# Performance work log

Hardware: AMD Instinct MI355X
Metric: run time of the kernel (lower is better)

Reference implementation:

```python
import jax, jax.numpy as jnp
import numpy as np

B, S, H, E, I_E, V = 4, 4096, 1024, 8, 512, 100000


def setup_inputs() -> dict:
    key = jax.random.key(0)
    k0, k1, k2, k3, k4, k5, k6 = jax.random.split(key, 7)
    hidden_states = jax.random.normal(k0, (B, S, H), dtype=jnp.float32)
    token_ids = jax.random.randint(k1, (B, S), 0, V, dtype=jnp.int64)
    mu = jax.random.normal(k2, (B, S, H), dtype=jnp.float32)
    # torch Linear(in,out,bias=False) weight is [out,in]; we store transposed [in,out]
    w_gate = jax.random.normal(k3, (E, H, I_E), dtype=jnp.float32) * 0.02
    w_up = jax.random.normal(k4, (E, H, I_E), dtype=jnp.float32) * 0.02
    w_down = jax.random.normal(k5, (E, I_E, H), dtype=jnp.float32) * 0.02
    # module zero-inits mu_router; use small random so the mu-override path is exercised
    mu_router_w = jax.random.normal(k6, (E, H), dtype=jnp.float32) * 0.02
    return {
        "hidden_states": hidden_states,
        "token_ids": token_ids,
        "mu": mu,
        "w_gate": w_gate,
        "w_up": w_up,
        "w_down": w_down,
        "mu_router_w": mu_router_w,
    }


def reference(hidden_states, token_ids, mu, w_gate, w_up, w_down, mu_router_w):
    num_experts = w_gate.shape[0]
    # deterministic token->expert mapping: token_id % num_experts (after clamp)
    tid = jnp.clip(token_ids, 0, V - 1)
    base_expert_ids = (tid % num_experts).astype(jnp.int32)  # [B,S]
    # mu-guided override: one_hot*10 + mu_logits, argmax
    mu_logits = jnp.einsum("bsh,eh->bse", mu, mu_router_w)
    base_one_hot = jax.nn.one_hot(base_expert_ids, num_experts, dtype=mu_logits.dtype)
    expert_ids = jnp.argmax(base_one_hot * 10.0 + mu_logits, axis=-1)  # [B,S]

    x = hidden_states.reshape(-1, H)          # [T,H], T=B*S
    eid = expert_ids.reshape(-1)              # [T]
    out = jnp.zeros_like(x)
    for e in range(num_experts):
        mask = (eid == e)[:, None]            # [T,1]
        g = x @ w_gate[e]                     # [T,I_E]
        u = x @ w_up[e]                       # [T,I_E]
        y = (jax.nn.silu(g) * u) @ w_down[e]  # [T,H] SwiGLU
        out = out + jnp.where(mask, y, 0.0)
    return out.reshape(hidden_states.shape)
```

## Files before the change

### kernel.cpp

```cpp
#include <hip/hip_runtime.h>
#include <stdint.h>

#define T_TOK   16384
#define H_DIM   1024
#define IE_DIM  512
#define E_NUM   8
#define V_MAX   100000

typedef __attribute__((ext_vector_type(8))) short bf16x8;
typedef __attribute__((ext_vector_type(4))) float f32x4;
typedef unsigned long long ull;

__device__ __forceinline__ unsigned short f2bf(float f) {
  union { float f; unsigned u; } v; v.f = f;
  unsigned r = v.u + 0x7fffu + ((v.u >> 16) & 1u);
  return (unsigned short)(r >> 16);
}

__device__ __forceinline__ void gload16(const void* g, void* l) {
  __builtin_amdgcn_global_load_lds(
      (const __attribute__((address_space(1))) unsigned int*)g,
      (__attribute__((address_space(3))) unsigned int*)(unsigned int)(uintptr_t)l,
      16, 0, 0);
}

__global__ __launch_bounds__(256) void k_route(
    const float* __restrict__ mu, const int* __restrict__ tok,
    const float* __restrict__ mrw, int* __restrict__ eid,
    int* __restrict__ blockCnt) {
  __shared__ int cnt[8];
  int tid = threadIdx.x;
  if (tid < 8) cnt[tid] = 0;
  int wv = blockIdx.x * 4 + (tid >> 6);
  int t0 = wv * 4;
  int lane = tid & 63;
  const float4* mrw4 = (const float4*)mrw;

  float acc[4][E_NUM];
#pragma unroll
  for (int i = 0; i < 4; i++)
#pragma unroll
    for (int e = 0; e < E_NUM; e++) acc[i][e] = 0.f;

#pragma unroll
  for (int j = 0; j < 4; j++) {
    int idx = lane + 64 * j;
    float4 wr[E_NUM];
#pragma unroll
    for (int e = 0; e < E_NUM; e++) wr[e] = mrw4[e * 256 + idx];
#pragma unroll
    for (int i = 0; i < 4; i++) {
      float4 m = ((const float4*)(mu + (size_t)(t0 + i) * H_DIM))[idx];
#pragma unroll
      for (int e = 0; e < E_NUM; e++)
        acc[i][e] += m.x * wr[e].x + m.y * wr[e].y + m.z * wr[e].z + m.w * wr[e].w;
    }
  }
#pragma unroll
  for (int i = 0; i < 4; i++)
#pragma unroll
    for (int e = 0; e < E_NUM; e++)
#pragma unroll
      for (int off = 32; off >= 1; off >>= 1)
        acc[i][e] += __shfl_xor(acc[i][e], off, 64);

  __syncthreads();
#pragma unroll
  for (int i = 0; i < 4; i++) {
    int tv = tok[t0 + i];
    if (tv < 0) tv = 0;
    if (tv > V_MAX - 1) tv = V_MAX - 1;
    int base = tv & 7;
    int best = 0; float bs = -1e30f;
#pragma unroll
    for (int e = 0; e < E_NUM; e++) {
      float s = acc[i][e] + (e == base ? 10.f : 0.f);
      if (s > bs) { bs = s; best = e; }
    }
    if (lane == i) {
      eid[t0 + i] = best;
      atomicAdd(&cnt[best], 1);
    }
  }
  __syncthreads();
  if (tid < 8) blockCnt[blockIdx.x * 8 + tid] = cnt[tid];
}

__global__ __launch_bounds__(1024) void k_scan2(
    const int* __restrict__ blockCnt, int* __restrict__ blockBase,
    int* __restrict__ offsets, int* __restrict__ tileOff) {
  int b = threadIdx.x;
  __shared__ ull s0[1024], s1[1024];
  __shared__ int offL[8];
  const int4* p = (const int4*)(blockCnt + b * 8);
  int4 x0 = p[0], x1 = p[1];
  int c[8] = {x0.x, x0.y, x0.z, x0.w, x1.x, x1.y, x1.z, x1.w};
  ull v0 = (ull)c[0] | ((ull)c[1] << 16) | ((ull)c[2] << 32) | ((ull)c[3] << 48);
  ull v1 = (ull)c[4] | ((ull)c[5] << 16) | ((ull)c[6] << 32) | ((ull)c[7] << 48);
  s0[b] = v0; s1[b] = v1;
  __syncthreads();
  for (int st = 1; st < 1024; st <<= 1) {
    ull a0 = 0, a1 = 0;
    if (b >= st) { a0 = s0[b - st]; a1 = s1[b - st]; }
    __syncthreads();
    v0 += a0; v1 += a1;
    s0[b] = v0; s1[b] = v1;
    __syncthreads();
  }
  if (b == 1023) {
    int tot[8];
#pragma unroll
    for (int e = 0; e < 4; e++) tot[e] = (int)((v0 >> (16 * e)) & 0xFFFF);
#pragma unroll
    for (int e = 0; e < 4; e++) tot[4 + e] = (int)((v1 >> (16 * e)) & 0xFFFF);
    int s = 0, ts = 0;
    for (int e = 0; e < E_NUM; e++) {
      offsets[e] = s; offL[e] = s; tileOff[e] = ts;
      s += tot[e];
      ts += (tot[e] + 127) >> 7;
    }
    offsets[E_NUM] = s; tileOff[E_NUM] = ts;
  }
  __syncthreads();
  int be[8];
#pragma unroll
  for (int e = 0; e < 4; e++)
    be[e] = offL[e] + (int)((v0 >> (16 * e)) & 0xFFFF) - c[e];
#pragma unroll
  for (int e = 0; e < 4; e++)
    be[4 + e] = offL[4 + e] + (int)((v1 >> (16 * e)) & 0xFFFF) - c[4 + e];
  int4* q = (int4*)(blockBase + b * 8);
  q[0] = make_int4(be[0], be[1], be[2], be[3]);
  q[1] = make_int4(be[4], be[5], be[6], be[7]);
}

__global__ __launch_bounds__(256) void k_gathtr(
    const float* __restrict__ hs, const int* __restrict__ eid,
    const int* __restrict__ blockBase, int* __restrict__ tokofrow,
    unsigned short* __restrict__ Xs,
    const float* __restrict__ wg, const float* __restrict__ wu,
    const float* __restrict__ wd, unsigned short* __restrict__ WgT,
    unsigned short* __restrict__ WuT, unsigned short* __restrict__ WdT) {
  __shared__ unsigned short lds[64][72];
  int tid = threadIdx.x;

  if (blockIdx.x < 1024) {
    int b = blockIdx.x;
    int* eL = (int*)&lds[0][0];
    int* posL = eL + 16;
    if (tid < 16) eL[tid] = eid[b * 16 + tid];
    __syncthreads();
    if (tid < 16) {
      int e = eL[tid];
      int r = 0;
      for (int j = 0; j < tid; j++) r += (eL[j] == e);
      int pos = blockBase[b * 8 + e] + r;
      posL[tid] = pos;
      tokofrow[pos] = b * 16 + tid;
    }
    __syncthreads();
    int w = tid >> 6, lane = tid & 63;
#pragma unroll
    for (int i = 0; i < 4; i++) {
      int li = w * 4 + i;
      int t = b * 16 + li;
      int pos = posL[li];
      const float4* src = (const float4*)(hs + (size_t)t * H_DIM);
      unsigned short* drow = Xs + (size_t)pos * H_DIM;
#pragma unroll
      for (int j = 0; j < 4; j++) {
        float4 v = src[lane + 64 * j];
        ushort4 bb;
        bb.x = f2bf(v.x); bb.y = f2bf(v.y); bb.z = f2bf(v.z); bb.w = f2bf(v.w);
        *(ushort4*)(drow + (lane + 64 * j) * 4) = bb;
      }
    }
  } else {
    int sel = (blockIdx.x - 1024) >> 10;
    int blk = blockIdx.x & 1023;
    const float* src; unsigned short* dst; int R, C;
    if (sel == 0)      { src = wg; dst = WgT; R = H_DIM; C = IE_DIM; }
    else if (sel == 1) { src = wu; dst = WuT; R = H_DIM; C = IE_DIM; }
    else               { src = wd; dst = WdT; R = IE_DIM; C = H_DIM; }
    int tpe = (R >> 6) * (C >> 6);
    int e = blk / tpe;
    int rem = blk % tpe;
    int tr = rem / (C >> 6);
    int tc = rem % (C >> 6);
    const float* s = src + (size_t)e * R * C;
    unsigned short* d = dst + (size_t)e * R * C;
    int r0 = tid >> 4;
    int c0 = (tid & 15) * 4;
#pragma unroll
    for (int i = 0; i < 4; i++) {
      int r = r0 + i * 16;
      float4 v = *(const float4*)(s + (size_t)(tr * 64 + r) * C + tc * 64 + c0);
      lds[r][c0 + 0] = f2bf(v.x); lds[r][c0 + 1] = f2bf(v.y);
      lds[r][c0 + 2] = f2bf(v.z); lds[r][c0 + 3] = f2bf(v.w);
    }
    __syncthreads();
    int oc = tid >> 2;
    int ob = (tid & 3) * 16;
    unsigned short tmp[16];
#pragma unroll
    for (int i = 0; i < 16; i++) tmp[i] = lds[ob + i][oc];
    uint4* dp = (uint4*)(d + (size_t)(tc * 64 + oc) * R + tr * 64 + ob);
    dp[0] = ((uint4*)tmp)[0];
    dp[1] = ((uint4*)tmp)[1];
  }
}

__global__ __launch_bounds__(512) void k_gemm1(
    const unsigned short* __restrict__ Xs,
    const unsigned short* __restrict__ WgT,
    const unsigned short* __restrict__ WuT,
    unsigned short* __restrict__ Hb,
    const int* __restrict__ offsets, const int* __restrict__ tileOff) {
  int bid0 = blockIdx.x;
  int xcd = bid0 & 7, seq = bid0 >> 3;
  int wg = (xcd < 4 ? xcd * 68 : 272 + (xcd - 4) * 67) + seq;
  int nt = wg & 3;
  int mlin = wg >> 2;
  if (mlin >= tileOff[E_NUM]) return;
  int e = 0;
#pragma unroll
  for (int i = 1; i < E_NUM; i++)
    if (mlin >= tileOff[i]) e = i;
  int mtile = mlin - tileOff[e];
  int segStart = offsets[e], segEnd = offsets[e + 1];
  int M = segEnd - segStart;

  __shared__ unsigned short Alds[3][128 * 32];
  __shared__ unsigned short Bglds[3][128 * 32];
  __shared__ unsigned short Bulds[3][128 * 32];

  int tid = threadIdx.x;
  int lane = tid & 63;
  int w = tid >> 6;
  int wm = w >> 2;
  int wn = w & 3;

  f32x4 accg[4][2], accu[4][2];
#pragma unroll
  for (int i = 0; i < 4; i++)
#pragma unroll
    for (int j = 0; j < 2; j++) {
      accg[i][j] = (f32x4)(0.f);
      accu[i][j] = (f32x4)(0.f);
    }

  int sr = tid >> 2;
  int sc = tid & 3;
  int scc = sc ^ ((sr >> 1) & 3);
  int grow = mtile * 128 + sr;
  if (grow > M - 1) grow = M - 1;
  const unsigned short* Arow = Xs + (size_t)(segStart + grow) * H_DIM + scc * 8;
  const unsigned short* Bgrow =
      WgT + (size_t)e * IE_DIM * H_DIM + (size_t)(nt * 128 + sr) * H_DIM + scc * 8;
  const unsigned short* Burow =
      WuT + (size_t)e * IE_DIM * H_DIM + (size_t)(nt * 128 + sr) * H_DIM + scc * 8;

#define STAGE1(buf, k0)                                            \
  {                                                                \
    gload16(Arow + (k0), (char*)Alds[buf] + tid * 16);             \
    gload16(Bgrow + (k0), (char*)Bglds[buf] + tid * 16);           \
    gload16(Burow + (k0), (char*)Bulds[buf] + tid * 16);           \
  }

  int kc = lane >> 4;
  int arow[4], browv[2];
#pragma unroll
  for (int mf = 0; mf < 4; mf++) arow[mf] = wm * 64 + mf * 16 + (lane & 15);
#pragma unroll
  for (int nf = 0; nf < 2; nf++) browv[nf] = wn * 32 + nf * 16 + (lane & 15);

  const int NT = H_DIM / 32;
  STAGE1(0, 0);
  STAGE1(1, 32);

  int cur = 0;
  for (int t = 0; t < NT; t++) {
    asm volatile("s_waitcnt vmcnt(3)" ::: "memory");
    __builtin_amdgcn_s_barrier();
    __builtin_amdgcn_sched_barrier(0);
    int tn = t + 2; if (tn >= NT) tn -= NT;
    int nbuf = cur + 2; if (nbuf >= 3) nbuf -= 3;
    STAGE1(nbuf, tn * 32);

    bf16x8 a[4], bg[2], bu[2];
#pragma unroll
    for (int mf = 0; mf < 4; mf++) {
      int row = arow[mf];
      int byte = row * 64 + ((kc ^ ((row >> 1) & 3)) << 4);
      a[mf] = *(const bf16x8*)((const char*)Alds[cur] + byte);
    }
#pragma unroll
    for (int nf = 0; nf < 2; nf++) {
      int row = browv[nf];
      int byte = row * 64 + ((kc ^ ((row >> 1) & 3)) << 4);
      bg[nf] = *(const bf16x8*)((const char*)Bglds[cur] + byte);
      bu[nf] = *(const bf16x8*)((const char*)Bulds[cur] + byte);
    }
    __builtin_amdgcn_s_setprio(1);
#pragma unroll
    for (int mf = 0; mf < 4; mf++)
#pragma unroll
      for (int nf = 0; nf < 2; nf++) {
        accg[mf][nf] = __builtin_amdgcn_mfma_f32_16x16x32_bf16(
            a[mf], bg[nf], accg[mf][nf], 0, 0, 0);
        accu[mf][nf] = __builtin_amdgcn_mfma_f32_16x16x32_bf16(
            a[mf], bu[nf], accu[mf][nf], 0, 0, 0);
      }
    __builtin_amdgcn_s_setprio(0);
    cur = (cur + 1 == 3) ? 0 : cur + 1;
  }
#undef STAGE1
  asm volatile("s_waitcnt vmcnt(0)" ::: "memory");

  int rowBase = segStart + mtile * 128 + wm * 64;
#pragma unroll
  for (int mf = 0; mf < 4; mf++)
#pragma unroll
    for (int nf = 0; nf < 2; nf++) {
      int col = nt * 128 + wn * 32 + nf * 16 + (lane & 15);
#pragma unroll
      for (int j = 0; j < 4; j++) {
        int r = rowBase + mf * 16 + (lane >> 4) * 4 + j;
        if (r < segEnd) {
          float g = accg[mf][nf][j];
          float u = accu[mf][nf][j];
          float h = (g / (1.f + __expf(-g))) * u;
          Hb[(size_t)r * IE_DIM + col] = f2bf(h);
        }
      }
    }
}

__global__ __launch_bounds__(512) void k_gemm2(
    const unsigned short* __restrict__ Hb,
    const unsigned short* __restrict__ WdT,
    float* __restrict__ out,
    const int* __restrict__ offsets, const int* __restrict__ tileOff,
    const int* __restrict__ tokofrow) {
  int bid0 = blockIdx.x;
  int wg = (bid0 & 7) * 135 + (bid0 >> 3);
  int nt = wg & 7;
  int mlin = wg >> 3;
  if (mlin >= tileOff[E_NUM]) return;
  int e = 0;
#pragma unroll
  for (int i = 1; i < E_NUM; i++)
    if (mlin >= tileOff[i]) e = i;
  int mtile = mlin - tileOff[e];
  int segStart = offsets[e], segEnd = offsets[e + 1];
  int M = segEnd - segStart;

  __shared__ unsigned short Alds[3][128 * 32];
  __shared__ unsigned short Blds[3][128 * 32];

  int tid = threadIdx.x;
  int lane = tid & 63;
  int w = tid >> 6;
  int wm = w >> 2;
  int wn = w & 3;

  f32x4 acc[4][2];
#pragma unroll
  for (int i = 0; i < 4; i++)
#pragma unroll
    for (int j = 0; j < 2; j++) acc[i][j] = (f32x4)(0.f);

  int sr = tid >> 2;
  int sc = tid & 3;
  int scc = sc ^ ((sr >> 1) & 3);
  int grow = mtile * 128 + sr;
  if (grow > M - 1) grow = M - 1;
  const unsigned short* Arow = Hb + (size_t)(segStart + grow) * IE_DIM + scc * 8;
  const unsigned short* Brow =
      WdT + (size_t)e * H_DIM * IE_DIM + (size_t)(nt * 128 + sr) * IE_DIM + scc * 8;

#define STAGE2(buf, k0)                                            \
  {                                                                \
    gload16(Arow + (k0), (char*)Alds[buf] + tid * 16);             \
    gload16(Brow + (k0), (char*)Blds[buf] + tid * 16);             \
  }

  int kc = lane >> 4;
  int arow[4], browv[2];
#pragma unroll
  for (int mf = 0; mf < 4; mf++) arow[mf] = wm * 64 + mf * 16 + (lane & 15);
#pragma unroll
  for (int nf = 0; nf < 2; nf++) browv[nf] = wn * 32 + nf * 16 + (lane & 15);

  const int NT = IE_DIM / 32;
  STAGE2(0, 0);
  STAGE2(1, 32);

  int cur = 0;
  for (int t = 0; t < NT; t++) {
    asm volatile("s_waitcnt vmcnt(2)" ::: "memory");
    __builtin_amdgcn_s_barrier();
    __builtin_amdgcn_sched_barrier(0);
    int tn = t + 2; if (tn >= NT) tn -= NT;
    int nbuf = cur + 2; if (nbuf >= 3) nbuf -= 3;
    STAGE2(nbuf, tn * 32);

    bf16x8 a[4], b[2];
#pragma unroll
    for (int mf = 0; mf < 4; mf++) {
      int row = arow[mf];
      int byte = row * 64 + ((kc ^ ((row >> 1) & 3)) << 4);
      a[mf] = *(const bf16x8*)((const char*)Alds[cur] + byte);
    }
#pragma unroll
    for (int nf = 0; nf < 2; nf++) {
      int row = browv[nf];
      int byte = row * 64 + ((kc ^ ((row >> 1) & 3)) << 4);
      b[nf] = *(const bf16x8*)((const char*)Blds[cur] + byte);
    }
    __builtin_amdgcn_s_setprio(1);
#pragma unroll
    for (int mf = 0; mf < 4; mf++)
#pragma unroll
      for (int nf = 0; nf < 2; nf++)
        acc[mf][nf] = __builtin_amdgcn_mfma_f32_16x16x32_bf16(
            a[mf], b[nf], acc[mf][nf], 0, 0, 0);
    __builtin_amdgcn_s_setprio(0);
    cur = (cur + 1 == 3) ? 0 : cur + 1;
  }
#undef STAGE2
  asm volatile("s_waitcnt vmcnt(0)" ::: "memory");

  int rowBase = segStart + mtile * 128 + wm * 64;
#pragma unroll
  for (int mf = 0; mf < 4; mf++)
#pragma unroll
    for (int nf = 0; nf < 2; nf++) {
      int col = nt * 128 + wn * 32 + nf * 16 + (lane & 15);
#pragma unroll
      for (int j = 0; j < 4; j++) {
        int r = rowBase + mf * 16 + (lane >> 4) * 4 + j;
        if (r < segEnd) {
          int t = tokofrow[r];
          out[(size_t)t * H_DIM + col] = acc[mf][nf][j];
        }
      }
    }
}

#define WS_XS    ((size_t)0)
#define WS_WGT   ((size_t)33554432)
#define WS_WUT   ((size_t)41943040)
#define WS_WDT   ((size_t)50331648)
#define WS_HB    ((size_t)58720256)
#define WS_EID   ((size_t)75497472)
#define WS_TOK   ((size_t)75563008)
#define WS_OFF   ((size_t)75628544)
#define WS_BC    ((size_t)75629568)
#define WS_BB    ((size_t)75662336)

extern "C" void kernel_launch(void* const* d_in, const int* in_sizes, int n_in,
                              void* d_out, int out_size, void* d_ws, size_t ws_size,
                              hipStream_t stream) {
  const float* hs  = (const float*)d_in[0];
  const int*   tok = (const int*)d_in[1];
  const float* mu  = (const float*)d_in[2];
  const float* wg  = (const float*)d_in[3];
  const float* wu  = (const float*)d_in[4];
  const float* wd  = (const float*)d_in[5];
  const float* mrw = (const float*)d_in[6];
  float* out = (float*)d_out;
  char* ws = (char*)d_ws;

  unsigned short* Xs  = (unsigned short*)(ws + WS_XS);
  unsigned short* WgT = (unsigned short*)(ws + WS_WGT);
  unsigned short* WuT = (unsigned short*)(ws + WS_WUT);
  unsigned short* WdT = (unsigned short*)(ws + WS_WDT);
  unsigned short* Hb  = (unsigned short*)(ws + WS_HB);
  int* eid      = (int*)(ws + WS_EID);
  int* tokofrow = (int*)(ws + WS_TOK);
  int* offsets  = (int*)(ws + WS_OFF);
  int* tileOff  = offsets + 16;
  int* blockCnt = (int*)(ws + WS_BC);
  int* blockBase= (int*)(ws + WS_BB);

  k_route<<<1024, 256, 0, stream>>>(mu, tok, mrw, eid, blockCnt);
  k_scan2<<<1, 1024, 0, stream>>>(blockCnt, blockBase, offsets, tileOff);
  k_gathtr<<<4096, 256, 0, stream>>>(hs, eid, blockBase, tokofrow, Xs,
                                     wg, wu, wd, WgT, WuT, WdT);
  k_gemm1<<<135 * 4, 512, 0, stream>>>(Xs, WgT, WuT, Hb, offsets, tileOff);
  k_gemm2<<<135 * 8, 512, 0, stream>>>(Hb, WdT, out, offsets, tileOff, tokofrow);
}
```

Baseline: 154.6 us.

## Precompute routing ranks in router and batch four weight-transpose tiles per block

The router kernel now computes each token's within-block rank and writes it to a workspace array, so the gather kernel no longer needs two LDS barriers and a serial rank loop before copying rows. The weight-transpose part now processes four 64x64 tiles per block with double-buffered LDS, loading the next tile's global data while the current one is stored. This cuts the grid from 4096 to 1792 blocks and overlaps loads with stores. The cost is more registers and LDS per block, plus an extra rank buffer write and read.

New measurement: 160.1 us. 3.6% more time.

```diff
diff --git a/kernel.cpp b/kernel.cpp
--- a/kernel.cpp
+++ b/kernel.cpp
@@ -27,8 +27,9 @@
 __global__ __launch_bounds__(256) void k_route(
     const float* __restrict__ mu, const int* __restrict__ tok,
     const float* __restrict__ mrw, int* __restrict__ eid,
-    int* __restrict__ blockCnt) {
+    int* __restrict__ rank, int* __restrict__ blockCnt) {
   __shared__ int cnt[8];
+  __shared__ int eL[16];
   int tid = threadIdx.x;
   if (tid < 8) cnt[tid] = 0;
   int wv = blockIdx.x * 4 + (tid >> 6);
@@ -79,10 +80,17 @@
     }
     if (lane == i) {
       eid[t0 + i] = best;
+      eL[(tid >> 6) * 4 + i] = best;
       atomicAdd(&cnt[best], 1);
     }
   }
   __syncthreads();
+  if (tid < 16) {
+    int e = eL[tid];
+    int r = 0;
+    for (int j = 0; j < tid; j++) r += (eL[j] == e);
+    rank[blockIdx.x * 16 + tid] = r;
+  }
   if (tid < 8) blockCnt[blockIdx.x * 8 + tid] = cnt[tid];
 }
 
@@ -134,37 +142,43 @@
   q[1] = make_int4(be[4], be[5], be[6], be[7]);
 }
 
+__device__ __forceinline__ void tr_bases(
+    int g, const float* wg, const float* wu, const float* wd,
+    unsigned short* WgT, unsigned short* WuT, unsigned short* WdT,
+    const float*& s, unsigned short*& d, int& C, int& R) {
+  int sel = g >> 10, blk = g & 1023;
+  const float* src; unsigned short* dst;
+  if (sel == 0)      { src = wg; dst = WgT; R = H_DIM; C = IE_DIM; }
+  else if (sel == 1) { src = wu; dst = WuT; R = H_DIM; C = IE_DIM; }
+  else               { src = wd; dst = WdT; R = IE_DIM; C = H_DIM; }
+  int tpe = (R >> 6) * (C >> 6);
+  int e = blk / tpe;
+  int rem = blk % tpe;
+  int tr = rem / (C >> 6);
+  int tc = rem % (C >> 6);
+  s = src + (size_t)e * R * C + (size_t)(tr * 64) * C + tc * 64;
+  d = dst + (size_t)e * R * C + (size_t)(tc * 64) * R + tr * 64;
+}
+
 __global__ __launch_bounds__(256) void k_gathtr(
     const float* __restrict__ hs, const int* __restrict__ eid,
-    const int* __restrict__ blockBase, int* __restrict__ tokofrow,
-    unsigned short* __restrict__ Xs,
+    const int* __restrict__ rank, const int* __restrict__ blockBase,
+    int* __restrict__ tokofrow, unsigned short* __restrict__ Xs,
     const float* __restrict__ wg, const float* __restrict__ wu,
     const float* __restrict__ wd, unsigned short* __restrict__ WgT,
     unsigned short* __restrict__ WuT, unsigned short* __restrict__ WdT) {
-  __shared__ unsigned short lds[64][72];
   int tid = threadIdx.x;
 
   if (blockIdx.x < 1024) {
     int b = blockIdx.x;
-    int* eL = (int*)&lds[0][0];
-    int* posL = eL + 16;
-    if (tid < 16) eL[tid] = eid[b * 16 + tid];
-    __syncthreads();
-    if (tid < 16) {
-      int e = eL[tid];
-      int r = 0;
-      for (int j = 0; j < tid; j++) r += (eL[j] == e);
-      int pos = blockBase[b * 8 + e] + r;
-      posL[tid] = pos;
-      tokofrow[pos] = b * 16 + tid;
-    }
-    __syncthreads();
     int w = tid >> 6, lane = tid & 63;
 #pragma unroll
     for (int i = 0; i < 4; i++) {
       int li = w * 4 + i;
       int t = b * 16 + li;
-      int pos = posL[li];
+      int e = eid[t];
+      int pos = blockBase[b * 8 + e] + rank[t];
+      if (lane == 0) tokofrow[pos] = t;
       const float4* src = (const float4*)(hs + (size_t)t * H_DIM);
       unsigned short* drow = Xs + (size_t)pos * H_DIM;
 #pragma unroll
@@ -176,37 +190,53 @@
       }
     }
   } else {
-    int sel = (blockIdx.x - 1024) >> 10;
-    int blk = blockIdx.x & 1023;
-    const float* src; unsigned short* dst; int R, C;
-    if (sel == 0)      { src = wg; dst = WgT; R = H_DIM; C = IE_DIM; }
-    else if (sel == 1) { src = wu; dst = WuT; R = H_DIM; C = IE_DIM; }
-    else               { src = wd; dst = WdT; R = IE_DIM; C = H_DIM; }
-    int tpe = (R >> 6) * (C >> 6);
-    int e = blk / tpe;
-    int rem = blk % tpe;
-    int tr = rem / (C >> 6);
-    int tc = rem % (C >> 6);
-    const float* s = src + (size_t)e * R * C;
-    unsigned short* d = dst + (size_t)e * R * C;
-    int r0 = tid >> 4;
-    int c0 = (tid & 15) * 4;
-#pragma unroll
-    for (int i = 0; i < 4; i++) {
-      int r = r0 + i * 16;
-      float4 v = *(const float4*)(s + (size_t)(tr * 64 + r) * C + tc * 64 + c0);
-      lds[r][c0 + 0] = f2bf(v.x); lds[r][c0 + 1] = f2bf(v.y);
-      lds[r][c0 + 2] = f2bf(v.z); lds[r][c0 + 3] = f2bf(v.w);
-    }
+    __shared__ unsigned short lds[2][64][72];
+    int base = (blockIdx.x - 1024) * 4;
+    int r0 = tid >> 4, c0 = (tid & 15) * 4;
+    int oc = tid >> 2, ob = (tid & 3) * 16;
+    float4 v0[4], v1[4];
+    unsigned short* dS[2]; int RS[2];
+
+#define TLOAD(g, vv, slot)                                                  \
+  { const float* s_; unsigned short* d_; int C_, R_;                        \
+    tr_bases(g, wg, wu, wd, WgT, WuT, WdT, s_, d_, C_, R_);                 \
+    _Pragma("unroll") for (int i = 0; i < 4; i++)                           \
+      vv[i] = *(const float4*)(s_ + (size_t)(r0 + i * 16) * C_ + c0);       \
+    dS[slot] = d_; RS[slot] = R_; }
+
+#define TWRITE(buf, vv)                                                     \
+  { _Pragma("unroll") for (int i = 0; i < 4; i++) {                         \
+      int r_ = r0 + i * 16;                                                 \
+      lds[buf][r_][c0 + 0] = f2bf(vv[i].x);                                 \
+      lds[buf][r_][c0 + 1] = f2bf(vv[i].y);                                 \
+      lds[buf][r_][c0 + 2] = f2bf(vv[i].z);                                 \
+      lds[buf][r_][c0 + 3] = f2bf(vv[i].w); } }
+
+#define TSTORE(buf, slot)                                                   \
+  { unsigned short tmp[16];                                                 \
+    _Pragma("unroll") for (int i = 0; i < 16; i++) tmp[i] = lds[buf][ob + i][oc]; \
+    uint4* dp_ = (uint4*)(dS[slot] + (size_t)oc * RS[slot] + ob);           \
+    dp_[0] = ((uint4*)tmp)[0]; dp_[1] = ((uint4*)tmp)[1]; }
+
+    TLOAD(base + 0, v0, 0);
+    TWRITE(0, v0);
+    TLOAD(base + 1, v1, 1);
     __syncthreads();
-    int oc = tid >> 2;
-    int ob = (tid & 3) * 16;
-    unsigned short tmp[16];
-#pragma unroll
-    for (int i = 0; i < 16; i++) tmp[i] = lds[ob + i][oc];
-    uint4* dp = (uint4*)(d + (size_t)(tc * 64 + oc) * R + tr * 64 + ob);
-    dp[0] = ((uint4*)tmp)[0];
-    dp[1] = ((uint4*)tmp)[1];
+    TSTORE(0, 0);
+    TWRITE(1, v1);
+    TLOAD(base + 2, v0, 0);
+    __syncthreads();
+    TSTORE(1, 1);
+    TWRITE(0, v0);
+    TLOAD(base + 3, v1, 1);
+    __syncthreads();
+    TSTORE(0, 0);
+    TWRITE(1, v1);
+    __syncthreads();
+    TSTORE(1, 1);
+#undef TLOAD
+#undef TWRITE
+#undef TSTORE
   }
 }
 
@@ -458,6 +488,7 @@
 #define WS_OFF   ((size_t)75628544)
 #define WS_BC    ((size_t)75629568)
 #define WS_BB    ((size_t)75662336)
+#define WS_RK    ((size_t)75695104)
 
 extern "C" void kernel_launch(void* const* d_in, const int* in_sizes, int n_in,
                               void* d_out, int out_size, void* d_ws, size_t ws_size,
@@ -483,10 +514,11 @@
   int* tileOff  = offsets + 16;
   int* blockCnt = (int*)(ws + WS_BC);
   int* blockBase= (int*)(ws + WS_BB);
-
-  k_route<<<1024, 256, 0, stream>>>(mu, tok, mrw, eid, blockCnt);
+  int* rank     = (int*)(ws + WS_RK);
+
+  k_route<<<1024, 256, 0, stream>>>(mu, tok, mrw, eid, rank, blockCnt);
   k_scan2<<<1, 1024, 0, stream>>>(blockCnt, blockBase, offsets, tileOff);
-  k_gathtr<<<4096, 256, 0, stream>>>(hs, eid, blockBase, tokofrow, Xs,
+  k_gathtr<<<1792, 256, 0, stream>>>(hs, eid, rank, blockBase, tokofrow, Xs,
                                      wg, wu, wd, WgT, WuT, WdT);
   k_gemm1<<<135 * 4, 512, 0, stream>>>(Xs, WgT, WuT, Hb, offsets, tileOff);
   k_gemm2<<<135 * 8, 512, 0, stream>>>(Hb, WdT, out, offsets, tileOff, tokofrow);
```

## Move down-projection weight transpose into gemm1 launch as extra blocks

Applied to the files above, without the earlier changes.

The fp32-to-bf16 transpose of w_down no longer runs in the gather/transpose kernel. It now runs in 512 extra blocks appended to the gemm1 grid, each handling two 64x64 tiles and reusing gemm1's LDS pool. The aim is to shorten the gather kernel and let the WdT conversion overlap with gemm1's tail or fill idle CUs. The cost is a larger gemm1 grid whose extra blocks compete with GEMM blocks for CUs, and the blocks must be scheduled well for any gain to appear.

Result: faster. 150.9 us (-2.4%).

```diff
diff --git a/kernel.cpp b/kernel.cpp
--- a/kernel.cpp
+++ b/kernel.cpp
@@ -139,8 +139,7 @@
     const int* __restrict__ blockBase, int* __restrict__ tokofrow,
     unsigned short* __restrict__ Xs,
     const float* __restrict__ wg, const float* __restrict__ wu,
-    const float* __restrict__ wd, unsigned short* __restrict__ WgT,
-    unsigned short* __restrict__ WuT, unsigned short* __restrict__ WdT) {
+    unsigned short* __restrict__ WgT, unsigned short* __restrict__ WuT) {
   __shared__ unsigned short lds[64][72];
   int tid = threadIdx.x;
 
@@ -178,10 +177,10 @@
   } else {
     int sel = (blockIdx.x - 1024) >> 10;
     int blk = blockIdx.x & 1023;
-    const float* src; unsigned short* dst; int R, C;
-    if (sel == 0)      { src = wg; dst = WgT; R = H_DIM; C = IE_DIM; }
-    else if (sel == 1) { src = wu; dst = WuT; R = H_DIM; C = IE_DIM; }
-    else               { src = wd; dst = WdT; R = IE_DIM; C = H_DIM; }
+    const float* src; unsigned short* dst;
+    const int R = H_DIM, C = IE_DIM;
+    if (sel == 0) { src = wg; dst = WgT; }
+    else          { src = wu; dst = WuT; }
     int tpe = (R >> 6) * (C >> 6);
     int e = blk / tpe;
     int rem = blk % tpe;
@@ -215,50 +214,53 @@
     const unsigned short* __restrict__ WgT,
     const unsigned short* __restrict__ WuT,
     unsigned short* __restrict__ Hb,
-    const int* __restrict__ offsets, const int* __restrict__ tileOff) {
-  int bid0 = blockIdx.x;
-  int xcd = bid0 & 7, seq = bid0 >> 3;
-  int wg = (xcd < 4 ? xcd * 68 : 272 + (xcd - 4) * 67) + seq;
-  int nt = wg & 3;
-  int mlin = wg >> 2;
-  if (mlin >= tileOff[E_NUM]) return;
-  int e = 0;
-#pragma unroll
-  for (int i = 1; i < E_NUM; i++)
-    if (mlin >= tileOff[i]) e = i;
-  int mtile = mlin - tileOff[e];
-  int segStart = offsets[e], segEnd = offsets[e + 1];
-  int M = segEnd - segStart;
-
+    const int* __restrict__ offsets, const int* __restrict__ tileOff,
+    const float* __restrict__ wd, unsigned short* __restrict__ WdT) {
   __shared__ unsigned short Alds[3][128 * 32];
   __shared__ unsigned short Bglds[3][128 * 32];
   __shared__ unsigned short Bulds[3][128 * 32];
 
+  int bid0 = blockIdx.x;
   int tid = threadIdx.x;
-  int lane = tid & 63;
-  int w = tid >> 6;
-  int wm = w >> 2;
-  int wn = w & 3;
-
-  f32x4 accg[4][2], accu[4][2];
-#pragma unroll
-  for (int i = 0; i < 4; i++)
-#pragma unroll
-    for (int j = 0; j < 2; j++) {
-      accg[i][j] = (f32x4)(0.f);
-      accu[i][j] = (f32x4)(0.f);
-    }
-
-  int sr = tid >> 2;
-  int sc = tid & 3;
-  int scc = sc ^ ((sr >> 1) & 3);
-  int grow = mtile * 128 + sr;
-  if (grow > M - 1) grow = M - 1;
-  const unsigned short* Arow = Xs + (size_t)(segStart + grow) * H_DIM + scc * 8;
-  const unsigned short* Bgrow =
-      WgT + (size_t)e * IE_DIM * H_DIM + (size_t)(nt * 128 + sr) * H_DIM + scc * 8;
-  const unsigned short* Burow =
-      WuT + (size_t)e * IE_DIM * H_DIM + (size_t)(nt * 128 + sr) * H_DIM + scc * 8;
+
+  if (bid0 < 540) {
+    int xcd = bid0 & 7, seq = bid0 >> 3;
+    int wg = (xcd < 4 ? xcd * 68 : 272 + (xcd - 4) * 67) + seq;
+    int nt = wg & 3;
+    int mlin = wg >> 2;
+    if (mlin < tileOff[E_NUM]) {
+      int e = 0;
+#pragma unroll
+      for (int i = 1; i < E_NUM; i++)
+        if (mlin >= tileOff[i]) e = i;
+      int mtile = mlin - tileOff[e];
+      int segStart = offsets[e], segEnd = offsets[e + 1];
+      int M = segEnd - segStart;
+
+      int lane = tid & 63;
+      int w = tid >> 6;
+      int wm = w >> 2;
+      int wn = w & 3;
+
+      f32x4 accg[4][2], accu[4][2];
+#pragma unroll
+      for (int i = 0; i < 4; i++)
+#pragma unroll
+        for (int j = 0; j < 2; j++) {
+          accg[i][j] = (f32x4)(0.f);
+          accu[i][j] = (f32x4)(0.f);
+        }
+
+      int sr = tid >> 2;
+      int sc = tid & 3;
+      int scc = sc ^ ((sr >> 1) & 3);
+      int grow = mtile * 128 + sr;
+      if (grow > M - 1) grow = M - 1;
+      const unsigned short* Arow = Xs + (size_t)(segStart + grow) * H_DIM + scc * 8;
+      const unsigned short* Bgrow =
+          WgT + (size_t)e * IE_DIM * H_DIM + (size_t)(nt * 128 + sr) * H_DIM + scc * 8;
+      const unsigned short* Burow =
+          WuT + (size_t)e * IE_DIM * H_DIM + (size_t)(nt * 128 + sr) * H_DIM + scc * 8;
 
 #define STAGE1(buf, k0)                                            \
   {                                                                \
@@ -267,73 +269,106 @@
     gload16(Burow + (k0), (char*)Bulds[buf] + tid * 16);           \
   }
 
-  int kc = lane >> 4;
-  int arow[4], browv[2];
-#pragma unroll
-  for (int mf = 0; mf < 4; mf++) arow[mf] = wm * 64 + mf * 16 + (lane & 15);
-#pragma unroll
-  for (int nf = 0; nf < 2; nf++) browv[nf] = wn * 32 + nf * 16 + (lane & 15);
-
-  const int NT = H_DIM / 32;
-  STAGE1(0, 0);
-  STAGE1(1, 32);
-
-  int cur = 0;
-  for (int t = 0; t < NT; t++) {
-    asm volatile("s_waitcnt vmcnt(3)" ::: "memory");
-    __builtin_amdgcn_s_barrier();
-    __builtin_amdgcn_sched_barrier(0);
-    int tn = t + 2; if (tn >= NT) tn -= NT;
-    int nbuf = cur + 2; if (nbuf >= 3) nbuf -= 3;
-    STAGE1(nbuf, tn * 32);
-
-    bf16x8 a[4], bg[2], bu[2];
-#pragma unroll
-    for (int mf = 0; mf < 4; mf++) {
-      int row = arow[mf];
-      int byte = row * 64 + ((kc ^ ((row >> 1) & 3)) << 4);
-      a[mf] = *(const bf16x8*)((const char*)Alds[cur] + byte);
-    }
-#pragma unroll
-    for (int nf = 0; nf < 2; nf++) {
-      int row = browv[nf];
-      int byte = row * 64 + ((kc ^ ((row >> 1) & 3)) << 4);
-      bg[nf] = *(const bf16x8*)((const char*)Bglds[cur] + byte);
-      bu[nf] = *(const bf16x8*)((const char*)Bulds[cur] + byte);
-    }
-    __builtin_amdgcn_s_setprio(1);
-#pragma unroll
-    for (int mf = 0; mf < 4; mf++)
-#pragma unroll
-      for (int nf = 0; nf < 2; nf++) {
-        accg[mf][nf] = __builtin_amdgcn_mfma_f32_16x16x32_bf16(
-            a[mf], bg[nf], accg[mf][nf], 0, 0, 0);
-        accu[mf][nf] = __builtin_amdgcn_mfma_f32_16x16x32_bf16(
-            a[mf], bu[nf], accu[mf][nf], 0, 0, 0);
+      int kc = lane >> 4;
+      int arow[4], browv[2];
+#pragma unroll
+      for (int mf = 0; mf < 4; mf++) arow[mf] = wm * 64 + mf * 16 + (lane & 15);
+#pragma unroll
+      for (int nf = 0; nf < 2; nf++) browv[nf] = wn * 32 + nf * 16 + (lane & 15);
+
+      const int NT = H_DIM / 32;
+      STAGE1(0, 0);
+      STAGE1(1, 32);
+
+      int cur = 0;
+      for (int t = 0; t < NT; t++) {
+        asm volatile("s_waitcnt vmcnt(3)" ::: "memory");
+        __builtin_amdgcn_s_barrier();
+        __builtin_amdgcn_sched_barrier(0);
+        int tn = t + 2; if (tn >= NT) tn -= NT;
+        int nbuf = cur + 2; if (nbuf >= 3) nbuf -= 3;
+        STAGE1(nbuf, tn * 32);
+
+        bf16x8 a[4], bg[2], bu[2];
+#pragma unroll
+        for (int mf = 0; mf < 4; mf++) {
+          int row = arow[mf];
+          int byte = row * 64 + ((kc ^ ((row >> 1) & 3)) << 4);
+          a[mf] = *(const bf16x8*)((const char*)Alds[cur] + byte);
+        }
+#pragma unroll
+        for (int nf = 0; nf < 2; nf++) {
+          int row = browv[nf];
+          int byte = row * 64 + ((kc ^ ((row >> 1) & 3)) << 4);
+          bg[nf] = *(const bf16x8*)((const char*)Bglds[cur] + byte);
+          bu[nf] = *(const bf16x8*)((const char*)Bulds[cur] + byte);
+        }
+        __builtin_amdgcn_s_setprio(1);
+#pragma unroll
+        for (int mf = 0; mf < 4; mf++)
+#pragma unroll
+          for (int nf = 0; nf < 2; nf++) {
+            accg[mf][nf] = __builtin_amdgcn_mfma_f32_16x16x32_bf16(
+                a[mf], bg[nf], accg[mf][nf], 0, 0, 0);
+            accu[mf][nf] = __builtin_amdgcn_mfma_f32_16x16x32_bf16(
+                a[mf], bu[nf], accu[mf][nf], 0, 0, 0);
+          }
+        __builtin_amdgcn_s_setprio(0);
+        cur = (cur + 1 == 3) ? 0 : cur + 1;
       }
-    __builtin_amdgcn_s_setprio(0);
-    cur = (cur + 1 == 3) ? 0 : cur + 1;
-  }
 #undef STAGE1
-  asm volatile("s_waitcnt vmcnt(0)" ::: "memory");
-
-  int rowBase = segStart + mtile * 128 + wm * 64;
-#pragma unroll
-  for (int mf = 0; mf < 4; mf++)
-#pragma unroll
-    for (int nf = 0; nf < 2; nf++) {
-      int col = nt * 128 + wn * 32 + nf * 16 + (lane & 15);
-#pragma unroll
-      for (int j = 0; j < 4; j++) {
-        int r = rowBase + mf * 16 + (lane >> 4) * 4 + j;
-        if (r < segEnd) {
-          float g = accg[mf][nf][j];
-          float u = accu[mf][nf][j];
-          float h = (g / (1.f + __expf(-g))) * u;
-          Hb[(size_t)r * IE_DIM + col] = f2bf(h);
+      asm volatile("s_waitcnt vmcnt(0)" ::: "memory");
+
+      int rowBase = segStart + mtile * 128 + wm * 64;
+#pragma unroll
+      for (int mf = 0; mf < 4; mf++)
+#pragma unroll
+        for (int nf = 0; nf < 2; nf++) {
+          int col = nt * 128 + wn * 32 + nf * 16 + (lane & 15);
+#pragma unroll
+          for (int j = 0; j < 4; j++) {
+            int r = rowBase + mf * 16 + (lane >> 4) * 4 + j;
+            if (r < segEnd) {
+              float g = accg[mf][nf][j];
+              float u = accu[mf][nf][j];
+              float h = (g / (1.f + __expf(-g))) * u;
+              Hb[(size_t)r * IE_DIM + col] = f2bf(h);
+            }
+          }
         }
-      }
-    }
+    }
+  } else {
+    unsigned short* pool = (unsigned short*)Alds;
+    int sub = tid >> 8;
+    int stid = tid & 255;
+    int g = (bid0 - 540) * 2 + sub;
+    int e2 = g >> 7;
+    int rem = g & 127;
+    int tr = rem >> 4;
+    int tc = rem & 15;
+    const float* s = wd + (size_t)e2 * IE_DIM * H_DIM + (size_t)(tr * 64) * H_DIM + tc * 64;
+    unsigned short* d = WdT + (size_t)e2 * IE_DIM * H_DIM + (size_t)(tc * 64) * IE_DIM + tr * 64;
+    unsigned short* lds72 = pool + sub * 4608;
+    int r0 = stid >> 4, c0 = (stid & 15) * 4;
+#pragma unroll
+    for (int i = 0; i < 4; i++) {
+      int r = r0 + i * 16;
+      float4 v = *(const float4*)(s + (size_t)r * H_DIM + c0);
+      lds72[r * 72 + c0 + 0] = f2bf(v.x);
+      lds72[r * 72 + c0 + 1] = f2bf(v.y);
+      lds72[r * 72 + c0 + 2] = f2bf(v.z);
+      lds72[r * 72 + c0 + 3] = f2bf(v.w);
+    }
+    __syncthreads();
+    int oc = stid >> 2;
+    int ob = (stid & 3) * 16;
+    unsigned short tmp[16];
+#pragma unroll
+    for (int i = 0; i < 16; i++) tmp[i] = lds72[(ob + i) * 72 + oc];
+    uint4* dp = (uint4*)(d + (size_t)oc * IE_DIM + ob);
+    dp[0] = ((uint4*)tmp)[0];
+    dp[1] = ((uint4*)tmp)[1];
+  }
 }
 
 __global__ __launch_bounds__(512) void k_gemm2(
@@ -486,8 +521,8 @@
 
   k_route<<<1024, 256, 0, stream>>>(mu, tok, mrw, eid, blockCnt);
   k_scan2<<<1, 1024, 0, stream>>>(blockCnt, blockBase, offsets, tileOff);
-  k_gathtr<<<4096, 256, 0, stream>>>(hs, eid, blockBase, tokofrow, Xs,
-                                     wg, wu, wd, WgT, WuT, WdT);
-  k_gemm1<<<135 * 4, 512, 0, stream>>>(Xs, WgT, WuT, Hb, offsets, tileOff);
+  k_gathtr<<<3072, 256, 0, stream>>>(hs, eid, blockBase, tokofrow, Xs,
+                                     wg, wu, WgT, WuT);
+  k_gemm1<<<1052, 512, 0, stream>>>(Xs, WgT, WuT, Hb, offsets, tileOff, wd, WdT);
   k_gemm2<<<135 * 8, 512, 0, stream>>>(Hb, WdT, out, offsets, tileOff, tokofrow);
 }
```
